# Performance work log

Measured on AMD Instinct MI355X. Metric: run time of the kernel, lower is better.

The kernel has to match this reference:

```python
import jax, jax.numpy as jnp
import numpy as np

B, T, V, NS, L, G, H = 16, 256, 18000, 30, 10, 3, 400


def setup_inputs() -> dict:
    key = jax.random.key(0)
    ks = jax.random.split(key, 12)
    return {
        'encoded_hidden': jax.random.normal(ks[0], (1, B, H), jnp.float32),
        'encoded_outputs': jax.random.normal(ks[1], (B, T, H), jnp.float32),
        'emb_weight': jax.random.normal(ks[2], (V, H), jnp.float32) * 0.02,
        'gru_w_ih': jax.random.normal(ks[3], (3 * H, H), jnp.float32) * 0.05,
        'gru_w_hh': jax.random.normal(ks[4], (3 * H, H), jnp.float32) * 0.05,
        'gru_b_ih': jnp.zeros((3 * H,), jnp.float32),
        'gru_b_hh': jnp.zeros((3 * H,), jnp.float32),
        'w_ratio': jax.random.normal(ks[5], (1, 3 * H), jnp.float32) * 0.05,
        'b_ratio': jnp.zeros((1,), jnp.float32),
        'w_gate': jax.random.normal(ks[6], (G, H), jnp.float32) * 0.05,
        'b_gate': jnp.zeros((G,), jnp.float32),
        'slot_emb': jax.random.normal(ks[7], (2 * NS, H), jnp.float32) * 0.1,
        'encoded_lens': jax.random.randint(ks[8], (B,), T // 2, T + 1, jnp.int32),
        'story': jax.random.randint(ks[9], (B, T), 0, V, jnp.int32),
        'target_batches': jax.random.randint(ks[10], (B, NS, L), 0, V, jnp.int32),
        'domain_idx': 2 * jnp.arange(NS, dtype=jnp.int32),
        'slotname_idx': 2 * jnp.arange(NS, dtype=jnp.int32) + 1,
    }


def _forward(encoded_hidden, encoded_outputs, emb_weight, gru_w_ih, gru_w_hh,
             gru_b_ih, gru_b_hh, w_ratio, b_ratio, w_gate, b_gate, slot_emb,
             encoded_lens, story, target_batches, domain_idx, slotname_idx):
    b, t, h = encoded_outputs.shape
    ns, l = target_batches.shape[1], target_batches.shape[2]
    n = ns * b  # flattened slot-major rows: row = slot*b + batch

    combined = slot_emb[domain_idx] + slot_emb[slotname_idx]          # (NS,H)
    dec_in0 = jnp.repeat(combined, b, axis=0)                          # (N,H)
    h0 = jnp.tile(encoded_hidden[0], (ns, 1))                          # (N,H)
    enc = jnp.tile(encoded_outputs, (ns, 1, 1))                        # (N,T,H)
    story_rep = jnp.tile(story, (ns, 1))                               # (N,T)
    lens_rep = jnp.tile(encoded_lens, ns)                              # (N,)
    mask = jnp.arange(t)[None, :] < lens_rep[:, None]                  # (N,T)
    rows = jnp.arange(n)[:, None]

    # teacher forcing: decoder input at step wi>=1 is emb of target at wi-1
    tgt = jnp.transpose(target_batches, (2, 1, 0)).reshape(l, n)       # (L,N)
    dec_inputs = jnp.concatenate([dec_in0[None], emb_weight[tgt[:-1]]], axis=0)

    def step(hid, x):
        gi = x @ gru_w_ih.T + gru_b_ih
        gh = hid @ gru_w_hh.T + gru_b_hh
        i_r, i_z, i_n = jnp.split(gi, 3, axis=-1)
        h_r, h_z, h_n = jnp.split(gh, 3, axis=-1)
        r = jax.nn.sigmoid(i_r + h_r)
        z = jax.nn.sigmoid(i_z + h_z)
        nn_ = jnp.tanh(i_n + r * h_n)
        h_new = (1.0 - z) * nn_ + z * hid                              # (N,H)
        # attend over encoder outputs
        scores = jnp.einsum('nh,nth->nt', h_new, enc)
        scores = jnp.where(mask, scores, -1e9)
        prob = jax.nn.softmax(scores, axis=1)                          # (N,T)
        context = jnp.einsum('nt,nth->nh', prob, enc)                  # (N,H)
        # vocab distribution
        p_vocab = jax.nn.softmax(h_new @ emb_weight.T, axis=1)         # (N,V)
        # pointer-generator mix
        p_gen_vec = jnp.concatenate([h_new, context, x], axis=-1)      # (N,3H)
        switch = jax.nn.sigmoid(p_gen_vec @ w_ratio.T + b_ratio)       # (N,1)
        p_ctx = jnp.zeros_like(p_vocab).at[rows, story_rep].add(prob)  # scatter-add
        final = (1.0 - switch) * p_ctx + switch * p_vocab              # (N,V)
        return h_new, (final, context)

    _, (finals, contexts) = jax.lax.scan(step, h0, dec_inputs)
    points = finals.reshape(l, ns, b, -1).transpose(1, 2, 0, 3)        # (NS,B,L,V)
    gates = (contexts[0] @ w_gate.T + b_gate).reshape(ns, b, -1)       # (NS,B,G)
    return points, gates


def reference(encoded_hidden, encoded_outputs, emb_weight, gru_w_ih, gru_w_hh,
              gru_b_ih, gru_b_hh, w_ratio, b_ratio, w_gate, b_gate, slot_emb,
              encoded_lens, story, target_batches, domain_idx, slotname_idx):
    return _forward(encoded_hidden, encoded_outputs, emb_weight, gru_w_ih,
                    gru_w_hh, gru_b_ih, gru_b_hh, w_ratio, b_ratio, w_gate,
                    b_gate, slot_emb, encoded_lens, story, target_batches,
                    domain_idx, slotname_idx)
```

## Files before the change

### kernel.cpp

```cpp
#include <hip/hip_runtime.h>
#include <hip/hip_bf16.h>

#define Bq 16
#define Tq 256
#define Vq 18000
#define NSq 30
#define Lq 10
#define Gq 3
#define Hq 400
#define Nq (NSq * Bq)
#define H3q (3 * Hq)
#define CHq 9000

typedef __bf16 bf16;
typedef __bf16 bf16x4 __attribute__((ext_vector_type(4)));
typedef __bf16 bf16x8 __attribute__((ext_vector_type(8)));
typedef float floatx16 __attribute__((ext_vector_type(16)));

__global__ __launch_bounds__(256) void k_f2b4(
    const float* __restrict__ src, bf16* __restrict__ dst, const int n4)
{
    int i = blockIdx.x * 256 + threadIdx.x;
    if (i >= n4) return;
    const float4 v = ((const float4*)src)[i];
    bf16x4 o;
    o[0] = (bf16)v.x; o[1] = (bf16)v.y; o[2] = (bf16)v.z; o[3] = (bf16)v.w;
    ((bf16x4*)dst)[i] = o;
}

__global__ __launch_bounds__(256) void k_prep(
    const float* __restrict__ slot_emb, const int* __restrict__ dom,
    const int* __restrict__ slo, const bf16* __restrict__ embb,
    const int* __restrict__ tgt, const float* __restrict__ ehid,
    float* __restrict__ h, bf16* __restrict__ hb, bf16* __restrict__ xb,
    const int step)
{
    int i = blockIdx.x * 256 + threadIdx.x;
    if (i >= Nq * Hq) return;
    int n = i / Hq, k = i - n * Hq;
    int s = n / Bq, b = n & (Bq - 1);
    if (step == 0) {
        float v = slot_emb[dom[s] * Hq + k] + slot_emb[slo[s] * Hq + k];
        xb[i] = (bf16)v;
        float hv = ehid[b * Hq + k];
        h[i] = hv;
        hb[i] = (bf16)hv;
    } else {
        int tv = tgt[(b * NSq + s) * Lq + (step - 1)];
        xb[i] = embb[(size_t)tv * Hq + k];
    }
}

__global__ __launch_bounds__(256) void k_gru_gemm(
    const bf16* __restrict__ xb, const bf16* __restrict__ hb,
    const bf16* __restrict__ w_ih, const bf16* __restrict__ w_hh,
    float* __restrict__ gi, float* __restrict__ gh)
{
    const int ct = blockIdx.x;
    const int which = blockIdx.z;
    const int wave = threadIdx.x >> 6;
    const int lane = threadIdx.x & 63;
    const int g = blockIdx.y * 4 + wave;
    if (g >= 15) return;
    const bf16* A = which ? hb : xb;
    const bf16* W = which ? w_hh : w_ih;
    float* O = which ? gh : gi;
    const int m = lane & 31;
    const int kh = (lane >> 5) * 8;
    const int row = g * 32 + m;
    int col = ct * 32 + m;
    if (col >= H3q) col = H3q - 1;
    const bf16* Ap = A + row * Hq + kh;
    const bf16* Wp = W + col * Hq + kh;
    floatx16 acc;
    #pragma unroll
    for (int r = 0; r < 16; ++r) acc[r] = 0.f;
    for (int kt = 0; kt < 25; ++kt) {
        bf16x8 a = *(const bf16x8*)(Ap + kt * 16);
        bf16x8 w = *(const bf16x8*)(Wp + kt * 16);
        acc = __builtin_amdgcn_mfma_f32_32x32x16_bf16(a, w, acc, 0, 0, 0);
    }
    const int j = ct * 32 + (lane & 31);
    if (j < H3q) {
        const int rbase = g * 32 + 4 * (lane >> 5);
        #pragma unroll
        for (int r = 0; r < 16; ++r) {
            int rr = rbase + (r & 3) + 8 * (r >> 2);
            O[rr * H3q + j] = acc[r];
        }
    }
}

__global__ __launch_bounds__(256) void k_gru_attn(
    const float* __restrict__ gi, const float* __restrict__ gh,
    const float* __restrict__ b_ih, const float* __restrict__ b_hh,
    float* __restrict__ h, bf16* __restrict__ hb,
    const bf16* __restrict__ xb, const bf16* __restrict__ encb,
    const int* __restrict__ lens, const float* __restrict__ w_ratio,
    const float* __restrict__ b_ratio, const float* __restrict__ w_gate,
    const float* __restrict__ b_gate, float* __restrict__ prob,
    float* __restrict__ swp, float* __restrict__ out_gates, const int step)
{
    const int n = blockIdx.x;
    const int b = n & (Bq - 1);
    const int tid = threadIdx.x;
    __shared__ float s_h[Hq];
    __shared__ float s_c[Hq];
    __shared__ float s_p[Tq];
    __shared__ float s_red[4];

    const float* gin = gi + n * H3q;
    const float* ghn = gh + n * H3q;
    for (int k = tid; k < Hq; k += 256) {
        float ir = gin[k]          + b_ih[k];
        float hr = ghn[k]          + b_hh[k];
        float iz = gin[Hq + k]     + b_ih[Hq + k];
        float hz = ghn[Hq + k]     + b_hh[Hq + k];
        float in_ = gin[2*Hq + k]  + b_ih[2*Hq + k];
        float hn_ = ghn[2*Hq + k]  + b_hh[2*Hq + k];
        float r = 1.f / (1.f + __expf(-(ir + hr)));
        float z = 1.f / (1.f + __expf(-(iz + hz)));
        float nn = tanhf(in_ + r * hn_);
        float hp = h[n * Hq + k];
        float hv = (1.f - z) * nn + z * hp;
        s_h[k] = hv;
        h[n * Hq + k] = hv;
        hb[n * Hq + k] = (bf16)hv;
    }
    __syncthreads();

    const int t = tid;
    const bf16* erow = encb + (size_t)(b * Tq + t) * Hq;
    float sc = 0.f;
    #pragma unroll 5
    for (int kc = 0; kc < Hq / 8; ++kc) {
        bf16x8 e = *(const bf16x8*)(erow + kc * 8);
        #pragma unroll
        for (int j = 0; j < 8; ++j) sc += s_h[kc * 8 + j] * (float)e[j];
    }
    const int len = lens[b];
    float score = (t < len) ? sc : -1e9f;

    float mx = score;
    for (int off = 32; off > 0; off >>= 1) mx = fmaxf(mx, __shfl_xor(mx, off, 64));
    if ((tid & 63) == 0) s_red[tid >> 6] = mx;
    __syncthreads();
    mx = fmaxf(fmaxf(s_red[0], s_red[1]), fmaxf(s_red[2], s_red[3]));
    float ev = __expf(score - mx);
    float sm = ev;
    for (int off = 32; off > 0; off >>= 1) sm += __shfl_xor(sm, off, 64);
    __syncthreads();
    if ((tid & 63) == 0) s_red[tid >> 6] = sm;
    __syncthreads();
    sm = s_red[0] + s_red[1] + s_red[2] + s_red[3];
    float p = ev / sm;
    s_p[t] = p;
    prob[n * Tq + t] = p;
    __syncthreads();

    for (int k = tid; k < Hq; k += 256) {
        float c = 0.f;
        const bf16* ecol = encb + (size_t)b * Tq * Hq + k;
        for (int tt = 0; tt < Tq; ++tt) c += s_p[tt] * (float)ecol[tt * Hq];
        s_c[k] = c;
    }
    __syncthreads();

    float part = 0.f;
    for (int k = tid; k < Hq; k += 256) {
        part += w_ratio[k]        * s_h[k]
              + w_ratio[Hq + k]   * s_c[k]
              + w_ratio[2*Hq + k] * (float)xb[n * Hq + k];
    }
    for (int off = 32; off > 0; off >>= 1) part += __shfl_xor(part, off, 64);
    __syncthreads();
    if ((tid & 63) == 0) s_red[tid >> 6] = part;
    __syncthreads();
    if (tid == 0) {
        float tot = s_red[0] + s_red[1] + s_red[2] + s_red[3] + b_ratio[0];
        swp[n] = 1.f / (1.f + __expf(-tot));
    }

    if (step == 0) {
        for (int gg = 0; gg < Gq; ++gg) {
            float pg = 0.f;
            for (int k = tid; k < Hq; k += 256)
                pg += w_gate[gg * Hq + k] * s_c[k];
            for (int off = 32; off > 0; off >>= 1) pg += __shfl_xor(pg, off, 64);
            __syncthreads();
            if ((tid & 63) == 0) s_red[tid >> 6] = pg;
            __syncthreads();
            if (tid == 0)
                out_gates[n * Gq + gg] =
                    s_red[0] + s_red[1] + s_red[2] + s_red[3] + b_gate[gg];
        }
    }
}

__global__ __launch_bounds__(256) void k_vocab_gemm(
    const bf16* __restrict__ hb, const bf16* __restrict__ embb,
    float* __restrict__ logits)
{
    const int ct = blockIdx.x;
    const int wave = threadIdx.x >> 6;
    const int lane = threadIdx.x & 63;
    const int m = lane & 31;
    const int kh = (lane >> 5) * 8;
    int col = ct * 32 + m;
    if (col >= Vq) col = Vq - 1;
    const bf16* Ep = embb + (size_t)col * Hq + kh;
    floatx16 acc[4];
    #pragma unroll
    for (int i = 0; i < 4; ++i)
        #pragma unroll
        for (int r = 0; r < 16; ++r) acc[i][r] = 0.f;

    for (int kt = 0; kt < 25; ++kt) {
        bf16x8 e = *(const bf16x8*)(Ep + kt * 16);
        #pragma unroll
        for (int i = 0; i < 4; ++i) {
            int g = wave + 4 * i;
            if (g < 15) {
                bf16x8 a = *(const bf16x8*)(hb + (g * 32 + m) * Hq + kh + kt * 16);
                acc[i] = __builtin_amdgcn_mfma_f32_32x32x16_bf16(a, e, acc[i], 0, 0, 0);
            }
        }
    }
    const int j = ct * 32 + (lane & 31);
    if (j < Vq) {
        #pragma unroll
        for (int i = 0; i < 4; ++i) {
            int g = wave + 4 * i;
            if (g < 15) {
                const int rbase = g * 32 + 4 * (lane >> 5);
                #pragma unroll
                for (int r = 0; r < 16; ++r) {
                    int rr = rbase + (r & 3) + 8 * (r >> 2);
                    logits[(size_t)rr * Vq + j] = acc[i][r];
                }
            }
        }
    }
}

__global__ __launch_bounds__(512) void k_softmax_final(
    const float* __restrict__ logits, const float* __restrict__ prob,
    const float* __restrict__ swp, const int* __restrict__ story,
    float* __restrict__ out, const int step)
{
    __shared__ float s_chunk[CHq];
    __shared__ float s_red[8];
    __shared__ float s_red2[8];
    __shared__ float s_MS[2];
    const int n = blockIdx.x;
    const int b = n & (Bq - 1);
    const int tid = threadIdx.x;
    const float* lr = logits + (size_t)n * Vq;

    float m = -1e30f, s = 0.f;
    for (int v = tid; v < Vq; v += 512) {
        float x = lr[v];
        float nm = fmaxf(m, x);
        s = s * __expf(m - nm) + __expf(x - nm);
        m = nm;
    }
    for (int off = 32; off > 0; off >>= 1) {
        float om = __shfl_xor(m, off, 64);
        float os = __shfl_xor(s, off, 64);
        float nm = fmaxf(m, om);
        s = s * __expf(m - nm) + os * __expf(om - nm);
        m = nm;
    }
    if ((tid & 63) == 0) { s_red[tid >> 6] = m; s_red2[tid >> 6] = s; }
    __syncthreads();
    if (tid == 0) {
        float M = -1e30f;
        for (int i = 0; i < 8; ++i) M = fmaxf(M, s_red[i]);
        float S = 0.f;
        for (int i = 0; i < 8; ++i) S += s_red2[i] * __expf(s_red[i] - M);
        s_MS[0] = M; s_MS[1] = S;
    }
    __syncthreads();
    const float M = s_MS[0];
    const float swv = swp[n];
    const float scale = swv / s_MS[1];
    float* orow = out + ((size_t)n * Lq + step) * Vq;

    #pragma unroll
    for (int c = 0; c < 2; ++c) {
        const int c0 = c * CHq;
        for (int v = tid; v < CHq; v += 512)
            s_chunk[v] = __expf(lr[c0 + v] - M) * scale;
        __syncthreads();
        if (tid < Tq) {
            int idx = story[b * Tq + tid];
            if (idx >= c0 && idx < c0 + CHq) {
                float add = (1.f - swv) * prob[n * Tq + tid];
                atomicAdd(&s_chunk[idx - c0], add);
            }
        }
        __syncthreads();
        for (int v = tid; v < CHq; v += 512)
            orow[c0 + v] = s_chunk[v];
        __syncthreads();
    }
}

extern "C" void kernel_launch(void* const* d_in, const int* in_sizes, int n_in,
                              void* d_out, int out_size, void* d_ws, size_t ws_size,
                              hipStream_t stream)
{
    const float* ehid    = (const float*)d_in[0];
    const float* enc     = (const float*)d_in[1];
    const float* emb     = (const float*)d_in[2];
    const float* w_ih    = (const float*)d_in[3];
    const float* w_hh    = (const float*)d_in[4];
    const float* b_ih    = (const float*)d_in[5];
    const float* b_hh    = (const float*)d_in[6];
    const float* w_ratio = (const float*)d_in[7];
    const float* b_ratio = (const float*)d_in[8];
    const float* w_gate  = (const float*)d_in[9];
    const float* b_gate  = (const float*)d_in[10];
    const float* slot_emb= (const float*)d_in[11];
    const int*  lens     = (const int*)d_in[12];
    const int*  story    = (const int*)d_in[13];
    const int*  tgt      = (const int*)d_in[14];
    const int*  dom      = (const int*)d_in[15];
    const int*  slo      = (const int*)d_in[16];

    float* out = (float*)d_out;
    float* out_gates = out + (size_t)NSq * Bq * Lq * Vq;

    char* w = (char*)d_ws;
    size_t off = 0;
    auto alloc = [&](size_t bytes) -> void* {
        void* p = (void*)(w + off);
        off += (bytes + 255) & ~(size_t)255;
        return p;
    };
    bf16*  xb     = (bf16*)alloc((size_t)Nq * Hq * 2);
    bf16*  hb     = (bf16*)alloc((size_t)Nq * Hq * 2);
    float* h      = (float*)alloc((size_t)Nq * Hq * 4);
    float* gi     = (float*)alloc((size_t)Nq * H3q * 4);
    float* gh     = (float*)alloc((size_t)Nq * H3q * 4);
    float* prob   = (float*)alloc((size_t)Nq * Tq * 4);
    float* swp    = (float*)alloc((size_t)Nq * 4);
    float* logits = (float*)alloc((size_t)Nq * Vq * 4);
    bf16*  embb   = (bf16*)alloc((size_t)Vq * Hq * 2);
    bf16*  wbih   = (bf16*)alloc((size_t)H3q * Hq * 2);
    bf16*  wbhh   = (bf16*)alloc((size_t)H3q * Hq * 2);
    bf16*  encb   = (bf16*)alloc((size_t)Bq * Tq * Hq * 2);

    {
        int n4;
        n4 = (Vq * Hq) / 4;
        k_f2b4<<<dim3((n4 + 255) / 256), dim3(256), 0, stream>>>(emb, embb, n4);
        n4 = (H3q * Hq) / 4;
        k_f2b4<<<dim3((n4 + 255) / 256), dim3(256), 0, stream>>>(w_ih, wbih, n4);
        k_f2b4<<<dim3((n4 + 255) / 256), dim3(256), 0, stream>>>(w_hh, wbhh, n4);
        n4 = (Bq * Tq * Hq) / 4;
        k_f2b4<<<dim3((n4 + 255) / 256), dim3(256), 0, stream>>>(enc, encb, n4);
    }

    for (int step = 0; step < Lq; ++step) {
        k_prep<<<dim3((Nq * Hq + 255) / 256), dim3(256), 0, stream>>>(
            slot_emb, dom, slo, embb, tgt, ehid, h, hb, xb, step);
        k_gru_gemm<<<dim3(38, 4, 2), dim3(256), 0, stream>>>(
            xb, hb, wbih, wbhh, gi, gh);
        k_gru_attn<<<dim3(Nq), dim3(256), 0, stream>>>(
            gi, gh, b_ih, b_hh, h, hb, xb, encb, lens, w_ratio, b_ratio,
            w_gate, b_gate, prob, swp, out_gates, step);
        k_vocab_gemm<<<dim3(563), dim3(256), 0, stream>>>(hb, embb, logits);
        k_softmax_final<<<dim3(Nq), dim3(512), 0, stream>>>(
            logits, prob, swp, story, out, step);
    }
}
```

Measured before the change: 1.380 ms.

## Fuse input gather into GRU GEMM, compute softmax partials in vocab GEMM, batch final

Removes the per-step prep kernel by building the GRU input rows directly inside the GEMM (embedding gather or slot-embedding sum), and recomputes the switch input the same way in the attention kernel. The vocab GEMM epilogue now emits per-tile max/sum-exp partials, so the final kernel reads those partials instead of re-scanning every logit row. All steps' logits, probs and switches are stored to separate buffers, and one final kernel runs over all steps at the end. The cost is a much larger workspace (logits for all steps) and extra shuffle reductions in the GEMM epilogue.

Result: slower. 1.487 ms (+7.7%).

```diff
diff --git a/kernel.cpp b/kernel.cpp
--- a/kernel.cpp
+++ b/kernel.cpp
@@ -10,6 +10,7 @@
 #define Hq 400
 #define Nq (NSq * Bq)
 #define H3q (3 * Hq)
+#define NTv 563
 #define CHq 9000
 
 typedef __bf16 bf16;
@@ -28,33 +29,24 @@
     ((bf16x4*)dst)[i] = o;
 }
 
-__global__ __launch_bounds__(256) void k_prep(
-    const float* __restrict__ slot_emb, const int* __restrict__ dom,
-    const int* __restrict__ slo, const bf16* __restrict__ embb,
-    const int* __restrict__ tgt, const float* __restrict__ ehid,
-    float* __restrict__ h, bf16* __restrict__ hb, bf16* __restrict__ xb,
-    const int step)
+__global__ __launch_bounds__(256) void k_init(
+    const float* __restrict__ ehid, float* __restrict__ h, bf16* __restrict__ hb)
 {
     int i = blockIdx.x * 256 + threadIdx.x;
     if (i >= Nq * Hq) return;
     int n = i / Hq, k = i - n * Hq;
-    int s = n / Bq, b = n & (Bq - 1);
-    if (step == 0) {
-        float v = slot_emb[dom[s] * Hq + k] + slot_emb[slo[s] * Hq + k];
-        xb[i] = (bf16)v;
-        float hv = ehid[b * Hq + k];
-        h[i] = hv;
-        hb[i] = (bf16)hv;
-    } else {
-        int tv = tgt[(b * NSq + s) * Lq + (step - 1)];
-        xb[i] = embb[(size_t)tv * Hq + k];
-    }
+    int b = n & (Bq - 1);
+    float hv = ehid[b * Hq + k];
+    h[i] = hv;
+    hb[i] = (bf16)hv;
 }
 
 __global__ __launch_bounds__(256) void k_gru_gemm(
-    const bf16* __restrict__ xb, const bf16* __restrict__ hb,
+    const bf16* __restrict__ hb, const bf16* __restrict__ embb,
+    const float* __restrict__ slot_emb, const int* __restrict__ dom,
+    const int* __restrict__ slo, const int* __restrict__ tgt,
     const bf16* __restrict__ w_ih, const bf16* __restrict__ w_hh,
-    float* __restrict__ gi, float* __restrict__ gh)
+    float* __restrict__ gi, float* __restrict__ gh, const int step)
 {
     const int ct = blockIdx.x;
     const int which = blockIdx.z;
@@ -62,7 +54,6 @@
     const int lane = threadIdx.x & 63;
     const int g = blockIdx.y * 4 + wave;
     if (g >= 15) return;
-    const bf16* A = which ? hb : xb;
     const bf16* W = which ? w_hh : w_ih;
     float* O = which ? gh : gi;
     const int m = lane & 31;
@@ -70,13 +61,38 @@
     const int row = g * 32 + m;
     int col = ct * 32 + m;
     if (col >= H3q) col = H3q - 1;
-    const bf16* Ap = A + row * Hq + kh;
     const bf16* Wp = W + col * Hq + kh;
+
+    const bf16* Ap = hb + row * Hq + kh;
+    const float* pA0 = nullptr; const float* pA1 = nullptr;
+    if (which == 0) {
+        const int s = row >> 4, bb = row & (Bq - 1);
+        if (step == 0) {
+            pA0 = slot_emb + dom[s] * Hq + kh;
+            pA1 = slot_emb + slo[s] * Hq + kh;
+        } else {
+            const int tv = tgt[(bb * NSq + s) * Lq + (step - 1)];
+            Ap = embb + (size_t)tv * Hq + kh;
+        }
+    }
+
     floatx16 acc;
     #pragma unroll
     for (int r = 0; r < 16; ++r) acc[r] = 0.f;
     for (int kt = 0; kt < 25; ++kt) {
-        bf16x8 a = *(const bf16x8*)(Ap + kt * 16);
+        bf16x8 a;
+        if (which == 1 || step > 0) {
+            a = *(const bf16x8*)(Ap + kt * 16);
+        } else {
+            const float4 u0 = *(const float4*)(pA0 + kt * 16);
+            const float4 u1 = *(const float4*)(pA0 + kt * 16 + 4);
+            const float4 v0 = *(const float4*)(pA1 + kt * 16);
+            const float4 v1 = *(const float4*)(pA1 + kt * 16 + 4);
+            a[0] = (bf16)(u0.x + v0.x); a[1] = (bf16)(u0.y + v0.y);
+            a[2] = (bf16)(u0.z + v0.z); a[3] = (bf16)(u0.w + v0.w);
+            a[4] = (bf16)(u1.x + v1.x); a[5] = (bf16)(u1.y + v1.y);
+            a[6] = (bf16)(u1.z + v1.z); a[7] = (bf16)(u1.w + v1.w);
+        }
         bf16x8 w = *(const bf16x8*)(Wp + kt * 16);
         acc = __builtin_amdgcn_mfma_f32_32x32x16_bf16(a, w, acc, 0, 0, 0);
     }
@@ -95,7 +111,9 @@
     const float* __restrict__ gi, const float* __restrict__ gh,
     const float* __restrict__ b_ih, const float* __restrict__ b_hh,
     float* __restrict__ h, bf16* __restrict__ hb,
-    const bf16* __restrict__ xb, const bf16* __restrict__ encb,
+    const bf16* __restrict__ embb, const float* __restrict__ slot_emb,
+    const int* __restrict__ dom, const int* __restrict__ slo,
+    const int* __restrict__ tgt, const bf16* __restrict__ encb,
     const int* __restrict__ lens, const float* __restrict__ w_ratio,
     const float* __restrict__ b_ratio, const float* __restrict__ w_gate,
     const float* __restrict__ b_gate, float* __restrict__ prob,
@@ -103,6 +121,7 @@
 {
     const int n = blockIdx.x;
     const int b = n & (Bq - 1);
+    const int s = n >> 4;
     const int tid = threadIdx.x;
     __shared__ float s_h[Hq];
     __shared__ float s_c[Hq];
@@ -167,10 +186,20 @@
     __syncthreads();
 
     float part = 0.f;
-    for (int k = tid; k < Hq; k += 256) {
-        part += w_ratio[k]        * s_h[k]
-              + w_ratio[Hq + k]   * s_c[k]
-              + w_ratio[2*Hq + k] * (float)xb[n * Hq + k];
+    if (step == 0) {
+        const float* x0 = slot_emb + dom[s] * Hq;
+        const float* x1 = slot_emb + slo[s] * Hq;
+        for (int k = tid; k < Hq; k += 256)
+            part += w_ratio[k]        * s_h[k]
+                  + w_ratio[Hq + k]   * s_c[k]
+                  + w_ratio[2*Hq + k] * (float)(bf16)(x0[k] + x1[k]);
+    } else {
+        const int tv = tgt[(b * NSq + s) * Lq + (step - 1)];
+        const bf16* xr = embb + (size_t)tv * Hq;
+        for (int k = tid; k < Hq; k += 256)
+            part += w_ratio[k]        * s_h[k]
+                  + w_ratio[Hq + k]   * s_c[k]
+                  + w_ratio[2*Hq + k] * (float)xr[k];
     }
     for (int off = 32; off > 0; off >>= 1) part += __shfl_xor(part, off, 64);
     __syncthreads();
@@ -199,7 +228,7 @@
 
 __global__ __launch_bounds__(256) void k_vocab_gemm(
     const bf16* __restrict__ hb, const bf16* __restrict__ embb,
-    float* __restrict__ logits)
+    float* __restrict__ logits, float2* __restrict__ partials)
 {
     const int ct = blockIdx.x;
     const int wave = threadIdx.x >> 6;
@@ -227,51 +256,64 @@
         }
     }
     const int j = ct * 32 + (lane & 31);
-    if (j < Vq) {
-        #pragma unroll
-        for (int i = 0; i < 4; ++i) {
-            int g = wave + 4 * i;
-            if (g < 15) {
-                const int rbase = g * 32 + 4 * (lane >> 5);
+    const bool jv = (j < Vq);
+    #pragma unroll
+    for (int i = 0; i < 4; ++i) {
+        int g = wave + 4 * i;
+        if (g < 15) {
+            const int rbase = g * 32 + 4 * (lane >> 5);
+            #pragma unroll
+            for (int r = 0; r < 16; ++r) {
+                int rr = rbase + (r & 3) + 8 * (r >> 2);
+                float v = acc[i][r];
+                if (jv) logits[(size_t)rr * Vq + j] = v;
+                float tm = jv ? v : -1e30f;
                 #pragma unroll
-                for (int r = 0; r < 16; ++r) {
-                    int rr = rbase + (r & 3) + 8 * (r >> 2);
-                    logits[(size_t)rr * Vq + j] = acc[i][r];
-                }
+                for (int off = 16; off > 0; off >>= 1)
+                    tm = fmaxf(tm, __shfl_xor(tm, off, 64));
+                float te = jv ? __expf(v - tm) : 0.f;
+                #pragma unroll
+                for (int off = 16; off > 0; off >>= 1)
+                    te += __shfl_xor(te, off, 64);
+                if ((lane & 31) == 0)
+                    partials[(size_t)rr * NTv + ct] = make_float2(tm, te);
             }
         }
     }
 }
 
-__global__ __launch_bounds__(512) void k_softmax_final(
-    const float* __restrict__ logits, const float* __restrict__ prob,
-    const float* __restrict__ swp, const int* __restrict__ story,
-    float* __restrict__ out, const int step)
+__global__ __launch_bounds__(512) void k_final(
+    const float* __restrict__ logits, const float2* __restrict__ partials,
+    const float* __restrict__ prob, const float* __restrict__ swp,
+    const int* __restrict__ story, float* __restrict__ out)
 {
     __shared__ float s_chunk[CHq];
     __shared__ float s_red[8];
     __shared__ float s_red2[8];
     __shared__ float s_MS[2];
     const int n = blockIdx.x;
+    const int step = blockIdx.y;
     const int b = n & (Bq - 1);
     const int tid = threadIdx.x;
-    const float* lr = logits + (size_t)n * Vq;
-
-    float m = -1e30f, s = 0.f;
-    for (int v = tid; v < Vq; v += 512) {
-        float x = lr[v];
-        float nm = fmaxf(m, x);
-        s = s * __expf(m - nm) + __expf(x - nm);
+    const size_t row = (size_t)step * Nq + n;
+    const float* lr = logits + row * Vq;
+    const float2* pr = partials + row * NTv;
+
+    float m = -1e30f, ss = 0.f;
+    for (int ct = tid; ct < NTv; ct += 512) {
+        float2 p = pr[ct];
+        float nm = fmaxf(m, p.x);
+        ss = ss * __expf(m - nm) + p.y * __expf(p.x - nm);
         m = nm;
     }
     for (int off = 32; off > 0; off >>= 1) {
         float om = __shfl_xor(m, off, 64);
-        float os = __shfl_xor(s, off, 64);
+        float os = __shfl_xor(ss, off, 64);
         float nm = fmaxf(m, om);
-        s = s * __expf(m - nm) + os * __expf(om - nm);
+        ss = ss * __expf(m - nm) + os * __expf(om - nm);
         m = nm;
     }
-    if ((tid & 63) == 0) { s_red[tid >> 6] = m; s_red2[tid >> 6] = s; }
+    if ((tid & 63) == 0) { s_red[tid >> 6] = m; s_red2[tid >> 6] = ss; }
     __syncthreads();
     if (tid == 0) {
         float M = -1e30f;
@@ -282,7 +324,7 @@
     }
     __syncthreads();
     const float M = s_MS[0];
-    const float swv = swp[n];
+    const float swv = swp[row];
     const float scale = swv / s_MS[1];
     float* orow = out + ((size_t)n * Lq + step) * Vq;
 
@@ -295,7 +337,7 @@
         if (tid < Tq) {
             int idx = story[b * Tq + tid];
             if (idx >= c0 && idx < c0 + CHq) {
-                float add = (1.f - swv) * prob[n * Tq + tid];
+                float add = (1.f - swv) * prob[row * Tq + tid];
                 atomicAdd(&s_chunk[idx - c0], add);
             }
         }
@@ -338,18 +380,18 @@
         off += (bytes + 255) & ~(size_t)255;
         return p;
     };
-    bf16*  xb     = (bf16*)alloc((size_t)Nq * Hq * 2);
-    bf16*  hb     = (bf16*)alloc((size_t)Nq * Hq * 2);
-    float* h      = (float*)alloc((size_t)Nq * Hq * 4);
-    float* gi     = (float*)alloc((size_t)Nq * H3q * 4);
-    float* gh     = (float*)alloc((size_t)Nq * H3q * 4);
-    float* prob   = (float*)alloc((size_t)Nq * Tq * 4);
-    float* swp    = (float*)alloc((size_t)Nq * 4);
-    float* logits = (float*)alloc((size_t)Nq * Vq * 4);
-    bf16*  embb   = (bf16*)alloc((size_t)Vq * Hq * 2);
-    bf16*  wbih   = (bf16*)alloc((size_t)H3q * Hq * 2);
-    bf16*  wbhh   = (bf16*)alloc((size_t)H3q * Hq * 2);
-    bf16*  encb   = (bf16*)alloc((size_t)Bq * Tq * Hq * 2);
+    bf16*   hb       = (bf16*)alloc((size_t)Nq * Hq * 2);
+    float*  h        = (float*)alloc((size_t)Nq * Hq * 4);
+    float*  gi       = (float*)alloc((size_t)Nq * H3q * 4);
+    float*  gh       = (float*)alloc((size_t)Nq * H3q * 4);
+    float*  prob     = (float*)alloc((size_t)Lq * Nq * Tq * 4);
+    float*  swp      = (float*)alloc((size_t)Lq * Nq * 4);
+    float*  logits   = (float*)alloc((size_t)Lq * Nq * Vq * 4);
+    float2* partials = (float2*)alloc((size_t)Lq * Nq * NTv * 8);
+    bf16*   embb     = (bf16*)alloc((size_t)Vq * Hq * 2);
+    bf16*   wbih     = (bf16*)alloc((size_t)H3q * Hq * 2);
+    bf16*   wbhh     = (bf16*)alloc((size_t)H3q * Hq * 2);
+    bf16*   encb     = (bf16*)alloc((size_t)Bq * Tq * Hq * 2);
 
     {
         int n4;
@@ -360,18 +402,21 @@
         k_f2b4<<<dim3((n4 + 255) / 256), dim3(256), 0, stream>>>(w_hh, wbhh, n4);
         n4 = (Bq * Tq * Hq) / 4;
         k_f2b4<<<dim3((n4 + 255) / 256), dim3(256), 0, stream>>>(enc, encb, n4);
+        k_init<<<dim3((Nq * Hq + 255) / 256), dim3(256), 0, stream>>>(ehid, h, hb);
     }
 
     for (int step = 0; step < Lq; ++step) {
-        k_prep<<<dim3((Nq * Hq + 255) / 256), dim3(256), 0, stream>>>(
-            slot_emb, dom, slo, embb, tgt, ehid, h, hb, xb, step);
         k_gru_gemm<<<dim3(38, 4, 2), dim3(256), 0, stream>>>(
-            xb, hb, wbih, wbhh, gi, gh);
+            hb, embb, slot_emb, dom, slo, tgt, wbih, wbhh, gi, gh, step);
         k_gru_attn<<<dim3(Nq), dim3(256), 0, stream>>>(
-            gi, gh, b_ih, b_hh, h, hb, xb, encb, lens, w_ratio, b_ratio,
-            w_gate, b_gate, prob, swp, out_gates, step);
-        k_vocab_gemm<<<dim3(563), dim3(256), 0, stream>>>(hb, embb, logits);
-        k_softmax_final<<<dim3(Nq), dim3(512), 0, stream>>>(
-            logits, prob, swp, story, out, step);
-    }
-}
+            gi, gh, b_ih, b_hh, h, hb, embb, slot_emb, dom, slo, tgt, encb,
+            lens, w_ratio, b_ratio, w_gate, b_gate,
+            prob + (size_t)step * Nq * Tq, swp + (size_t)step * Nq,
+            out_gates, step);
+        k_vocab_gemm<<<dim3(NTv), dim3(256), 0, stream>>>(
+            hb, embb, logits + (size_t)step * Nq * Vq,
+            partials + (size_t)step * Nq * NTv);
+    }
+    k_final<<<dim3(Nq, Lq), dim3(512), 0, stream>>>(
+        logits, partials, prob, swp, story, out);
+}
```
